# Optimization experiments

Measured on AMD Instinct MI355X. Metric: run time of the kernel, lower is better.

Reference implementation:

```python
import jax, jax.numpy as jnp
import numpy as np

N_HEAD = 12
N_EMBED = 768

def setup_inputs() -> dict:
    key = jax.random.key(0)
    ks = jax.random.split(key, 5)
    B, T, C = 8, 1024, N_EMBED
    s_in = 1.0 / np.sqrt(C)
    s3 = 1.0 / np.sqrt(3 * C)
    return {
        "x": jax.random.normal(ks[0], (B, T, C), dtype=jnp.float32),
        "W_qkv": jax.random.normal(ks[1], (C, 3 * C), dtype=jnp.float32) * s_in,
        "b_qkv": jnp.zeros((3 * C,), dtype=jnp.float32),
        "W_out": jax.random.normal(ks[2], (C, C), dtype=jnp.float32) * s_in,
        "b_out": jnp.zeros((C,), dtype=jnp.float32),
    }

def reference(x, W_qkv, b_qkv, W_out, b_out):
    B, T, C = x.shape
    H = N_HEAD
    d_k = C // H
    qkv = x @ W_qkv + b_qkv  # [B,T,3C]
    q, k, v = jnp.split(qkv, 3, axis=-1)
    # [B,H,T,d]
    q = q.reshape(B, T, H, d_k).transpose(0, 2, 1, 3)
    k = k.reshape(B, T, H, d_k).transpose(0, 2, 1, 3)
    v = v.reshape(B, T, H, d_k).transpose(0, 2, 1, 3)
    logits = jnp.einsum('bhqd,bhkd->bhqk', q, k) * (d_k ** -0.5)
    causal = jnp.tril(jnp.ones((T, T), dtype=bool))
    logits = jnp.where(causal, logits, -jnp.inf)
    scores = jax.nn.softmax(logits, axis=-1)
    out = jnp.einsum('bhqk,bhkd->bhqd', scores, v)
    out = out.transpose(0, 2, 1, 3).reshape(B, T, C)
    return out @ W_out + b_out
```

## Files before the change

### kernel.cpp

```cpp
#include <hip/hip_runtime.h>
#include <stdint.h>

#define B_ 8
#define T_ 1024
#define C_ 768
#define H_ 12
#define DK 64
#define BT (B_*T_)
#define NQKV (3*C_)

typedef unsigned short u16;
typedef __bf16 bf16x8 __attribute__((ext_vector_type(8)));
typedef __bf16 bf16x4 __attribute__((ext_vector_type(4)));
typedef float  f32x4  __attribute__((ext_vector_type(4)));

typedef const __attribute__((address_space(1))) void gvoid_t;
typedef __attribute__((address_space(3))) void lvoid_t;

__device__ __forceinline__ void gl_lds16(const void* g, void* l) {
    __builtin_amdgcn_global_load_lds((gvoid_t*)g, (lvoid_t*)l, 16, 0, 0);
}

__device__ __forceinline__ u16 f2b(float f) {
    union { float f; unsigned int u; } v; v.f = f;
    unsigned int u = v.u;
    return (u16)((u + 0x7fffu + ((u >> 16) & 1u)) >> 16);
}

__device__ __forceinline__ f32x4 mfma16(bf16x8 a, bf16x8 b, f32x4 c) {
    return __builtin_amdgcn_mfma_f32_16x16x32_bf16(a, b, c, 0, 0, 0);
}

__global__ void k_convert(const float* __restrict__ in, u16* __restrict__ out, int n4) {
    int i = blockIdx.x * blockDim.x + threadIdx.x;
    if (i < n4) {
        float4 f = ((const float4*)in)[i];
        uint2 o;
        o.x = (unsigned)f2b(f.x) | ((unsigned)f2b(f.y) << 16);
        o.y = (unsigned)f2b(f.z) | ((unsigned)f2b(f.w) << 16);
        ((uint2*)out)[i] = o;
    }
}

__global__ __launch_bounds__(256)
void k_transpose_convert(const float* __restrict__ w, u16* __restrict__ wt,
                         int K, int N) {
    __shared__ u16 tile[32][34];
    const int tx = threadIdx.x, ty = threadIdx.y;
    const int n0 = blockIdx.x * 32, k0 = blockIdx.y * 32;
    #pragma unroll
    for (int i = 0; i < 4; i++)
        tile[ty + i * 8][tx] = f2b(w[(size_t)(k0 + ty + i * 8) * N + n0 + tx]);
    __syncthreads();
    #pragma unroll
    for (int i = 0; i < 4; i++)
        wt[(size_t)(n0 + ty + i * 8) * K + k0 + tx] = tile[tx][ty + i * 8];
}

template <int EPI>
__global__ __launch_bounds__(256)
void k_gemm(const u16* __restrict__ A, const u16* __restrict__ Bt,
            const float* __restrict__ bias,
            u16* __restrict__ qo, u16* __restrict__ ko, u16* __restrict__ vto,
            float* __restrict__ outf, int M, int N, int K)
{
    __shared__ u16 As[128 * 32];
    __shared__ u16 Bs[128 * 32];
    const int tid  = threadIdx.x;
    const int lane = tid & 63;
    const int w    = tid >> 6;
    const int quad = lane >> 4;
    const int col  = lane & 15;
    const int m0   = blockIdx.y * 128;
    const int n0   = blockIdx.x * 128;
    const int wm   = (w >> 1) * 64;
    const int wn   = (w & 1) * 64;

    f32x4 zero4 = {0.f, 0.f, 0.f, 0.f};
    f32x4 acc[4][4];
    #pragma unroll
    for (int i = 0; i < 4; i++)
        #pragma unroll
        for (int j = 0; j < 4; j++) acc[i][j] = zero4;

    const int sr  = tid >> 2;
    const int scc = (tid & 3) * 8;
    const u16* gA = A  + (size_t)(m0 + sr) * K + scc;
    const u16* gB = Bt + (size_t)(n0 + sr) * K + scc;
    char* ldsA0 = (char*)As + w * 1024;
    char* ldsA1 = (char*)As + 4096 + w * 1024;
    char* ldsB0 = (char*)Bs + w * 1024;
    char* ldsB1 = (char*)Bs + 4096 + w * 1024;

    for (int kt = 0; kt < K; kt += 32) {
        __syncthreads();
        gl_lds16(gA + kt,                  ldsA0);
        gl_lds16(gA + (size_t)64 * K + kt, ldsA1);
        gl_lds16(gB + kt,                  ldsB0);
        gl_lds16(gB + (size_t)64 * K + kt, ldsB1);
        __syncthreads();

        bf16x8 af[4], bfr[4];
        #pragma unroll
        for (int mt = 0; mt < 4; mt++)
            af[mt] = *(const bf16x8*)&As[(wm + mt * 16 + col) * 32 + quad * 8];
        #pragma unroll
        for (int nt = 0; nt < 4; nt++)
            bfr[nt] = *(const bf16x8*)&Bs[(wn + nt * 16 + col) * 32 + quad * 8];
        #pragma unroll
        for (int mt = 0; mt < 4; mt++)
            #pragma unroll
            for (int nt = 0; nt < 4; nt++)
                acc[mt][nt] = mfma16(af[mt], bfr[nt], acc[mt][nt]);
    }

    #pragma unroll
    for (int mt = 0; mt < 4; mt++) {
        #pragma unroll
        for (int nt = 0; nt < 4; nt++) {
            #pragma unroll
            for (int r = 0; r < 4; r++) {
                int m = m0 + wm + mt * 16 + quad * 4 + r;
                int n = n0 + wn + nt * 16 + col;
                float v = acc[mt][nt][r] + bias[n];
                if constexpr (EPI == 0) {
                    int sec = n / C_;
                    int c   = n - sec * C_;
                    int h   = c >> 6;
                    int d   = c & 63;
                    int b   = m >> 10;
                    int t   = m & 1023;
                    int bh  = b * H_ + h;
                    u16 bv  = f2b(v);
                    if (sec == 0)      qo [((size_t)bh * T_ + t) * DK + d] = bv;
                    else if (sec == 1) ko [((size_t)bh * T_ + t) * DK + d] = bv;
                    else               vto[((size_t)bh * DK + d) * T_ + t] = bv;
                } else {
                    outf[(size_t)m * N + n] = v;
                }
            }
        }
    }
}

#define PSTRIDE 72

__device__ __forceinline__ bf16x8 ld_sw(const u16* base, int row, int half,
                                        int quad, int c7) {
    return *(const bf16x8*)(base + row * DK + (((half * 4 + quad) ^ c7) * 8));
}

template <bool MASK>
__device__ __forceinline__ void attn_chunk(
    const u16* Ks, const u16* Vs, __bf16* pbuf,
    const bf16x8 (&qf)[2][2], bf16x8 ones,
    int kv0, int qw, int quad, int col,
    f32x4 (&oacc)[2][4], f32x4 (&lacc)[2])
{
    const int c7 = col & 7;
    f32x4 zero4 = {0.f, 0.f, 0.f, 0.f};
    f32x4 st[2][4];
    #pragma unroll
    for (int g = 0; g < 4; g++) {
        bf16x8 klo = ld_sw(Ks, g * 16 + col, 0, quad, c7);
        bf16x8 khi = ld_sw(Ks, g * 16 + col, 1, quad, c7);
        st[0][g] = mfma16(khi, qf[0][1], mfma16(klo, qf[0][0], zero4));
        st[1][g] = mfma16(khi, qf[1][1], mfma16(klo, qf[1][0], zero4));
    }
    const float scl = 0.18033688f;
    #pragma unroll
    for (int s = 0; s < 2; s++) {
        __bf16* pb = pbuf + s * 16 * PSTRIDE + col * PSTRIDE;
        #pragma unroll
        for (int g = 0; g < 4; g++) {
            bf16x4 pp;
            #pragma unroll
            for (int r = 0; r < 4; r++) {
                float p = __builtin_amdgcn_exp2f(st[s][g][r] * scl - 12.0f);
                if (MASK) {
                    int kv = kv0 + g * 16 + quad * 4 + r;
                    if (kv > qw + s * 16 + col) p = 0.f;
                }
                pp[r] = (__bf16)p;
            }
            *(bf16x4*)(pb + g * 16 + quad * 4) = pp;
        }
    }
    __builtin_amdgcn_s_waitcnt(0xc07f);
    bf16x8 pf[2][2];
    #pragma unroll
    for (int s = 0; s < 2; s++) {
        const __bf16* pb = pbuf + s * 16 * PSTRIDE + col * PSTRIDE;
        pf[s][0] = *(const bf16x8*)(pb + quad * 8);
        pf[s][1] = *(const bf16x8*)(pb + 32 + quad * 8);
        lacc[s] = mfma16(pf[s][1], ones, mfma16(pf[s][0], ones, lacc[s]));
    }
    #pragma unroll
    for (int dt = 0; dt < 4; dt++) {
        bf16x8 vlo = ld_sw(Vs, dt * 16 + col, 0, quad, c7);
        bf16x8 vhi = ld_sw(Vs, dt * 16 + col, 1, quad, c7);
        #pragma unroll
        for (int s = 0; s < 2; s++)
            oacc[s][dt] = mfma16(pf[s][1], vhi, mfma16(pf[s][0], vlo, oacc[s][dt]));
    }
}

__global__ __launch_bounds__(256, 4)
void k_attn(const u16* __restrict__ Q, const u16* __restrict__ Kf,
            const u16* __restrict__ Vt, u16* __restrict__ Of)
{
    __shared__ u16 Ks[64 * DK];
    __shared__ u16 Vs[64 * DK];
    __shared__ __bf16 Plds[4][32 * PSTRIDE];
    const int bh   = blockIdx.x;
    const int b    = bh / H_;
    const int h    = bh - b * H_;
    const int tid  = threadIdx.x;
    const int lane = tid & 63;
    const int w    = tid >> 6;
    const int quad = lane >> 4;
    const int col  = lane & 15;
    const int ty   = 7 - (int)blockIdx.y;
    const int nch  = 2 * ty + 2;
    const int qw   = ty * 128 + w * 32;
    __bf16* pbuf = Plds[w];

    const u16* Qb = Q  + (size_t)bh * T_ * DK;
    const u16* Kb = Kf + (size_t)bh * T_ * DK;
    const u16* Vb = Vt + (size_t)bh * DK * T_;

    int sG0 = tid, sG1 = 256 + tid;
    int sr0 = sG0 >> 3, sg0 = (sG0 & 7) ^ (sr0 & 7);
    int sr1 = sG1 >> 3, sg1 = (sG1 & 7) ^ (sr1 & 7);

    bf16x8 qf[2][2];
    #pragma unroll
    for (int s = 0; s < 2; s++) {
        const u16* qp = Qb + (size_t)(qw + s * 16 + col) * DK;
        qf[s][0] = *(const bf16x8*)(qp + quad * 8);
        qf[s][1] = *(const bf16x8*)(qp + 32 + quad * 8);
    }

    bf16x8 ones;
    #pragma unroll
    for (int i = 0; i < 8; i++) ((u16*)&ones)[i] = 0x3F80;

    f32x4 zero4 = {0.f, 0.f, 0.f, 0.f};
    f32x4 oacc[2][4];
    f32x4 lacc[2] = {zero4, zero4};
    #pragma unroll
    for (int s = 0; s < 2; s++)
        #pragma unroll
        for (int dt = 0; dt < 4; dt++) oacc[s][dt] = zero4;

    #pragma unroll 1
    for (int c = 0; c < nch; ++c) {
        const int kv0 = c * 64;
        __syncthreads();
        gl_lds16(Kb + (size_t)(kv0 + sr0) * DK + sg0 * 8, (char*)Ks + w * 1024);
        gl_lds16(Kb + (size_t)(kv0 + sr1) * DK + sg1 * 8, (char*)Ks + 4096 + w * 1024);
        gl_lds16(Vb + (size_t)sr0 * T_ + kv0 + sg0 * 8,   (char*)Vs + w * 1024);
        gl_lds16(Vb + (size_t)sr1 * T_ + kv0 + sg1 * 8,   (char*)Vs + 4096 + w * 1024);
        __syncthreads();

        if (kv0 <= qw + 31) {
            if (kv0 + 63 <= qw)
                attn_chunk<false>(Ks, Vs, pbuf, qf, ones, kv0, qw, quad, col, oacc, lacc);
            else
                attn_chunk<true>(Ks, Vs, pbuf, qf, ones, kv0, qw, quad, col, oacc, lacc);
        }
    }

    #pragma unroll
    for (int s = 0; s < 2; s++) {
        #pragma unroll
        for (int r = 0; r < 4; r++) {
            float inv = 1.f / lacc[s][r];
            int t = qw + s * 16 + quad * 4 + r;
            u16* op = Of + ((size_t)(b * T_ + t)) * C_ + h * DK;
            #pragma unroll
            for (int dt = 0; dt < 4; dt++) op[dt * 16 + col] = f2b(oacc[s][dt][r] * inv);
        }
    }
}

extern "C" void kernel_launch(void* const* d_in, const int* in_sizes, int n_in,
                              void* d_out, int out_size, void* d_ws, size_t ws_size,
                              hipStream_t stream) {
    const float* x    = (const float*)d_in[0];
    const float* Wqkv = (const float*)d_in[1];
    const float* bqkv = (const float*)d_in[2];
    const float* Wout = (const float*)d_in[3];
    const float* bout = (const float*)d_in[4];
    float* out = (float*)d_out;

    char* ws = (char*)d_ws;
    u16* xb    = (u16*)(ws);
    u16* wqkvT = (u16*)(ws + 12582912);
    u16* woutT = (u16*)(ws + 16121856);
    u16* qw    = (u16*)(ws + 17301504);
    u16* kw    = (u16*)(ws + 29884416);
    u16* vtw   = (u16*)(ws + 42467328);
    u16* aw    = (u16*)(ws + 55050240);

    k_convert<<<(BT * C_ / 4) / 256, 256, 0, stream>>>(x, xb, BT * C_ / 4);
    k_transpose_convert<<<dim3(NQKV / 32, C_ / 32), dim3(32, 8), 0, stream>>>(Wqkv, wqkvT, C_, NQKV);
    k_transpose_convert<<<dim3(C_ / 32, C_ / 32), dim3(32, 8), 0, stream>>>(Wout, woutT, C_, C_);

    k_gemm<0><<<dim3(NQKV / 128, BT / 128), 256, 0, stream>>>(
        xb, wqkvT, bqkv, qw, kw, vtw, nullptr, BT, NQKV, C_);

    k_attn<<<dim3(B_ * H_, 8), 256, 0, stream>>>(qw, kw, vtw, aw);

    k_gemm<1><<<dim3(C_ / 128, BT / 128), 256, 0, stream>>>(
        aw, woutT, bout, nullptr, nullptr, nullptr, out, BT, C_, C_);
}
```

Before: 210.7 us.

## Double-buffer LDS tiles in GEMM and attention with swizzled GEMM layout

Both the GEMM and attention kernels now keep two LDS buffers and prefetch the next K/V or A/B tile with global_load_lds before computing on the current one. Explicit barriers and vmcnt waits replace the paired __syncthreads, so global loads can overlap the MFMA work. The GEMM LDS layout also gets an XOR swizzle on the 16-byte column index to reduce bank conflicts on fragment reads. The cost is double the LDS footprint, and the attention kernel's occupancy hint drops from 4 to 3 blocks per CU.

```diff
diff --git a/kernel.cpp b/kernel.cpp
--- a/kernel.cpp
+++ b/kernel.cpp
@@ -16,6 +16,10 @@
 
 typedef const __attribute__((address_space(1))) void gvoid_t;
 typedef __attribute__((address_space(3))) void lvoid_t;
+
+#define WC_VM4   0xF74
+#define WC_VM0   0xF70
+#define WC_LGKM0 0xC07F
 
 __device__ __forceinline__ void gl_lds16(const void* g, void* l) {
     __builtin_amdgcn_global_load_lds((gvoid_t*)g, (lvoid_t*)l, 16, 0, 0);
@@ -64,8 +68,8 @@
             u16* __restrict__ qo, u16* __restrict__ ko, u16* __restrict__ vto,
             float* __restrict__ outf, int M, int N, int K)
 {
-    __shared__ u16 As[128 * 32];
-    __shared__ u16 Bs[128 * 32];
+    __shared__ u16 As[2][128 * 32];
+    __shared__ u16 Bs[2][128 * 32];
     const int tid  = threadIdx.x;
     const int lane = tid & 63;
     const int w    = tid >> 6;
@@ -84,35 +88,52 @@
         for (int j = 0; j < 4; j++) acc[i][j] = zero4;
 
     const int sr  = tid >> 2;
-    const int scc = (tid & 3) * 8;
+    const int scc = ((tid & 3) ^ ((sr >> 1) & 3)) * 8;
     const u16* gA = A  + (size_t)(m0 + sr) * K + scc;
     const u16* gB = Bt + (size_t)(n0 + sr) * K + scc;
-    char* ldsA0 = (char*)As + w * 1024;
-    char* ldsA1 = (char*)As + 4096 + w * 1024;
-    char* ldsB0 = (char*)Bs + w * 1024;
-    char* ldsB1 = (char*)Bs + 4096 + w * 1024;
-
-    for (int kt = 0; kt < K; kt += 32) {
-        __syncthreads();
-        gl_lds16(gA + kt,                  ldsA0);
-        gl_lds16(gA + (size_t)64 * K + kt, ldsA1);
-        gl_lds16(gB + kt,                  ldsB0);
-        gl_lds16(gB + (size_t)64 * K + kt, ldsB1);
-        __syncthreads();
-
+
+    const int NIT = K >> 5;
+
+    #define STAGE(kt, bufi)                                            \
+        do {                                                           \
+            gl_lds16(gA + (kt),                  (char*)As[bufi] + w * 1024);        \
+            gl_lds16(gA + (size_t)64 * K + (kt), (char*)As[bufi] + 4096 + w * 1024); \
+            gl_lds16(gB + (kt),                  (char*)Bs[bufi] + w * 1024);        \
+            gl_lds16(gB + (size_t)64 * K + (kt), (char*)Bs[bufi] + 4096 + w * 1024); \
+        } while (0)
+
+    STAGE(0, 0);
+    for (int it = 0; it < NIT; ++it) {
+        const int cur = it & 1;
+        __builtin_amdgcn_s_barrier();
+        if (it + 1 < NIT) {
+            STAGE((it + 1) << 5, cur ^ 1);
+            __builtin_amdgcn_s_waitcnt(WC_VM4);
+        } else {
+            __builtin_amdgcn_s_waitcnt(WC_VM0);
+        }
+        __builtin_amdgcn_s_barrier();
+
+        const u16* Ab = As[cur];
+        const u16* Bb = Bs[cur];
         bf16x8 af[4], bfr[4];
         #pragma unroll
-        for (int mt = 0; mt < 4; mt++)
-            af[mt] = *(const bf16x8*)&As[(wm + mt * 16 + col) * 32 + quad * 8];
-        #pragma unroll
-        for (int nt = 0; nt < 4; nt++)
-            bfr[nt] = *(const bf16x8*)&Bs[(wn + nt * 16 + col) * 32 + quad * 8];
+        for (int mt = 0; mt < 4; mt++) {
+            int row = wm + mt * 16 + col;
+            af[mt] = *(const bf16x8*)&Ab[row * 32 + ((quad ^ ((row >> 1) & 3)) * 8)];
+        }
+        #pragma unroll
+        for (int nt = 0; nt < 4; nt++) {
+            int row = wn + nt * 16 + col;
+            bfr[nt] = *(const bf16x8*)&Bb[row * 32 + ((quad ^ ((row >> 1) & 3)) * 8)];
+        }
         #pragma unroll
         for (int mt = 0; mt < 4; mt++)
             #pragma unroll
             for (int nt = 0; nt < 4; nt++)
                 acc[mt][nt] = mfma16(af[mt], bfr[nt], acc[mt][nt]);
     }
+    #undef STAGE
 
     #pragma unroll
     for (int mt = 0; mt < 4; mt++) {
@@ -186,7 +207,7 @@
             *(bf16x4*)(pb + g * 16 + quad * 4) = pp;
         }
     }
-    __builtin_amdgcn_s_waitcnt(0xc07f);
+    __builtin_amdgcn_s_waitcnt(WC_LGKM0);
     bf16x8 pf[2][2];
     #pragma unroll
     for (int s = 0; s < 2; s++) {
@@ -205,12 +226,12 @@
     }
 }
 
-__global__ __launch_bounds__(256, 4)
+__global__ __launch_bounds__(256, 3)
 void k_attn(const u16* __restrict__ Q, const u16* __restrict__ Kf,
             const u16* __restrict__ Vt, u16* __restrict__ Of)
 {
-    __shared__ u16 Ks[64 * DK];
-    __shared__ u16 Vs[64 * DK];
+    __shared__ u16 Ks[2][64 * DK];
+    __shared__ u16 Vs[2][64 * DK];
     __shared__ __bf16 Plds[4][32 * PSTRIDE];
     const int bh   = blockIdx.x;
     const int b    = bh / H_;
@@ -253,23 +274,37 @@
         #pragma unroll
         for (int dt = 0; dt < 4; dt++) oacc[s][dt] = zero4;
 
+    #define ASTAGE(c, bufi)                                                            \
+        do {                                                                           \
+            int kvs = (c) * 64;                                                        \
+            gl_lds16(Kb + (size_t)(kvs + sr0) * DK + sg0 * 8, (char*)Ks[bufi] + w * 1024);        \
+            gl_lds16(Kb + (size_t)(kvs + sr1) * DK + sg1 * 8, (char*)Ks[bufi] + 4096 + w * 1024); \
+            gl_lds16(Vb + (size_t)sr0 * T_ + kvs + sg0 * 8,   (char*)Vs[bufi] + w * 1024);        \
+            gl_lds16(Vb + (size_t)sr1 * T_ + kvs + sg1 * 8,   (char*)Vs[bufi] + 4096 + w * 1024); \
+        } while (0)
+
+    ASTAGE(0, 0);
     #pragma unroll 1
     for (int c = 0; c < nch; ++c) {
+        const int cur = c & 1;
+        __builtin_amdgcn_s_barrier();
+        if (c + 1 < nch) {
+            ASTAGE(c + 1, cur ^ 1);
+            __builtin_amdgcn_s_waitcnt(WC_VM4);
+        } else {
+            __builtin_amdgcn_s_waitcnt(WC_VM0);
+        }
+        __builtin_amdgcn_s_barrier();
+
         const int kv0 = c * 64;
-        __syncthreads();
-        gl_lds16(Kb + (size_t)(kv0 + sr0) * DK + sg0 * 8, (char*)Ks + w * 1024);
-        gl_lds16(Kb + (size_t)(kv0 + sr1) * DK + sg1 * 8, (char*)Ks + 4096 + w * 1024);
-        gl_lds16(Vb + (size_t)sr0 * T_ + kv0 + sg0 * 8,   (char*)Vs + w * 1024);
-        gl_lds16(Vb + (size_t)sr1 * T_ + kv0 + sg1 * 8,   (char*)Vs + 4096 + w * 1024);
-        __syncthreads();
-
         if (kv0 <= qw + 31) {
             if (kv0 + 63 <= qw)
-                attn_chunk<false>(Ks, Vs, pbuf, qf, ones, kv0, qw, quad, col, oacc, lacc);
+                attn_chunk<false>(Ks[cur], Vs[cur], pbuf, qf, ones, kv0, qw, quad, col, oacc, lacc);
             else
-                attn_chunk<true>(Ks, Vs, pbuf, qf, ones, kv0, qw, quad, col, oacc, lacc);
-        }
-    }
+                attn_chunk<true>(Ks[cur], Vs[cur], pbuf, qf, ones, kv0, qw, quad, col, oacc, lacc);
+        }
+    }
+    #undef ASTAGE
 
     #pragma unroll
     for (int s = 0; s < 2; s++) {
```

New measurement: 204.7 us. 1.03x faster.
